# Performance work log

Measured on AMD Instinct MI355X. Metric: run time of the kernel, lower is better.

## Reference

```python
import jax, jax.numpy as jnp
import numpy as np
from math import ceil

B, T, FQ, D = 2, 48, 100, 512
H, DFF, L, WSZ = 8, 2048, 6, 8


def setup_inputs() -> dict:
    key = jax.random.key(0)
    ks = jax.random.split(key, 8)
    g = lambda k, shape: jax.random.normal(k, shape, jnp.float32) * 0.02
    return {
        "frame_queries": jax.random.normal(ks[0], (B, T, FQ, D), jnp.float32),
        "Wp": g(ks[1], (D, D)), "bp": jnp.zeros((D,), jnp.float32),
        "Wqkv": g(ks[2], (L, 3 * D, D)), "bqkv": jnp.zeros((L, 3 * D), jnp.float32),
        "Wo": g(ks[3], (L, D, D)), "bo": jnp.zeros((L, D), jnp.float32),
        "ln1_s": jnp.ones((L, D), jnp.float32), "ln1_b": jnp.zeros((L, D), jnp.float32),
        "W1": g(ks[4], (L, DFF, D)), "b1": jnp.zeros((L, DFF), jnp.float32),
        "W2": g(ks[5], (L, D, DFF)), "b2": jnp.zeros((L, D), jnp.float32),
        "ln2_s": jnp.ones((L, D), jnp.float32), "ln2_b": jnp.zeros((L, D), jnp.float32),
    }


def _ln(x, s, b, eps=1e-5):
    mu = x.mean(-1, keepdims=True)
    var = ((x - mu) ** 2).mean(-1, keepdims=True)
    return (x - mu) * jax.lax.rsqrt(var + eps) * s + b


def _mha(x, Wqkv_i, bqkv_i, Wo_i, bo_i, add_mask):
    # x: [Bw, S, C]; add_mask: None or [Bw, 1, S, S] additive float
    Bw, S, C = x.shape
    hd = C // H
    qkv = x @ Wqkv_i.T + bqkv_i
    q, k, v = jnp.split(qkv, 3, axis=-1)
    q = q.reshape(Bw, S, H, hd).transpose(0, 2, 1, 3)
    k = k.reshape(Bw, S, H, hd).transpose(0, 2, 1, 3)
    v = v.reshape(Bw, S, H, hd).transpose(0, 2, 1, 3)
    scores = jnp.einsum('bhqd,bhkd->bhqk', q, k) * jnp.float32(1.0 / np.sqrt(hd))
    if add_mask is not None:
        scores = scores + add_mask
    a = jax.nn.softmax(scores, axis=-1)
    o = jnp.einsum('bhqk,bhkd->bhqd', a, v).transpose(0, 2, 1, 3).reshape(Bw, S, C)
    return o @ Wo_i.T + bo_i


def _shift_mask():
    # padding mask is all-False (T % WSZ == 0), faithful construction of the
    # shifted-window additive mask as in the torch code.
    Nw = T // WSZ
    half = int(ceil(WSZ / 2))
    S = WSZ * FQ
    am = jnp.zeros((B, T), dtype=bool)
    r = jnp.roll(am, half, axis=1).reshape(B, Nw, WSZ)
    m = jnp.broadcast_to(r[..., None], (B, Nw, WSZ, WSZ))
    m = m.at[:, 0].set(m[:, 0] | m[:, 0].swapaxes(-1, -2))
    m = m.at[:, -1].set(m[:, -1] | m[:, -1].swapaxes(-1, -2))
    m = m.at[:, 0, :half, half:].set(True)
    m = m.at[:, 0, half:, :half].set(True)
    mfull = jnp.broadcast_to(m.reshape(B * Nw, WSZ, 1, WSZ, 1),
                             (B * Nw, WSZ, FQ, WSZ, FQ)).reshape(B * Nw, S, S)
    return (mfull.astype(jnp.float32) * -1000.0)[:, None]  # [B*Nw,1,S,S]


def reference(frame_queries, Wp, bp, Wqkv, bqkv, Wo, bo, ln1_s, ln1_b,
              W1, b1, W2, b2, ln2_s, ln2_b):
    Nw = T // WSZ
    half = int(ceil(WSZ / 2))
    S = WSZ * FQ
    x = frame_queries @ Wp.T + bp  # [B, T, FQ, D]
    shift_add = _shift_mask()
    for i in range(L):
        if i % 2 == 0:
            # plain window attention
            xw = x.reshape(B * Nw, S, D)
            xw = _ln(xw + _mha(xw, Wqkv[i], bqkv[i], Wo[i], bo[i], None),
                     ln1_s[i], ln1_b[i])
            x = xw.reshape(B, T, FQ, D)
        else:
            # shifted window attention
            xs = jnp.roll(x, half, axis=1)
            xw = xs.reshape(B * Nw, S, D)
            xw = _ln(xw + _mha(xw, Wqkv[i], bqkv[i], Wo[i], bo[i], shift_add),
                     ln1_s[i], ln1_b[i])
            x = jnp.roll(xw.reshape(B, T, FQ, D), -half, axis=1)
        # FFN (pointwise over channel dim)
        h = jax.nn.relu(x @ W1[i].T + b1[i]) @ W2[i].T + b2[i]
        x = _ln(x + h, ln2_s[i], ln2_b[i])
    return x  # [B, T, FQ, D] == 'lb t nq c'
```

## Files before the change

### kernel.cpp

```cpp
#include <hip/hip_runtime.h>


typedef float  f4    __attribute__((ext_vector_type(4)));
typedef __bf16 bf8   __attribute__((ext_vector_type(8)));
typedef unsigned short u16x8 __attribute__((ext_vector_type(8)));
typedef unsigned short u16x4 __attribute__((ext_vector_type(4)));

__device__ __forceinline__ unsigned short f2bf(float f) {
    unsigned int u = __builtin_bit_cast(unsigned int, f);
    u += 0x7fffu + ((u >> 16) & 1u);
    return (unsigned short)(u >> 16);
}
__device__ __forceinline__ float bf2f(unsigned short s) {
    return __builtin_bit_cast(float, ((unsigned int)s) << 16);
}

#define GLD16(gp, lp) __builtin_amdgcn_global_load_lds( \
    (const __attribute__((address_space(1))) void*)(gp), \
    (__attribute__((address_space(3))) void*)(lp), 16, 0, 0)

__device__ __forceinline__ int map_row(int r, int rshift) {
    if (!rshift) return r;
    int bb = r / 4800, rem = r % 4800;
    int tt = rem / 100, f = rem - tt * 100;
    return bb * 4800 + ((tt + rshift) % 48) * 100 + f;
}

template<int BM>
__global__ __launch_bounds__(256) void mfma_gemm(
    const unsigned short* __restrict__ A, const unsigned short* __restrict__ W,
    const float* __restrict__ bias, float* Cf, unsigned short* Cb,
    int M, int N, int K, int relu, int rshift, int qscale, int NB)
{
    constexpr int MI      = BM / 32;
    constexpr int ABUF    = BM * 32;
    constexpr int SB      = ABUF + 4096;
    constexpr int AROUNDS = BM / 64;
    __shared__ unsigned short Ls[3 * SB];
    const int tid = threadIdx.x, lane = tid & 63, wave = tid >> 6;

    const int per = gridDim.x >> 3;
    const int l = (blockIdx.x & 7) * per + (blockIdx.x >> 3);
    if (l >= NB * (M / BM)) return;
    const int n0 = (l % NB) * 128, m0 = (l / NB) * BM;

    const unsigned short* ga[AROUNDS];
    #pragma unroll
    for (int it = 0; it < AROUNDS; ++it) {
        int s = it * 256 + tid, row = s >> 2, cg = (s & 3) ^ ((row >> 1) & 3);
        ga[it] = A + (size_t)map_row(m0 + row, rshift) * K + cg * 8;
    }
    const unsigned short* gb[2];
    #pragma unroll
    for (int it = 0; it < 2; ++it) {
        int s = it * 256 + tid, row = s >> 2, cg = (s & 3) ^ ((row >> 1) & 3);
        gb[it] = W + (size_t)(n0 + row) * K + cg * 8;
    }

    const int wm = (wave >> 1) * (BM / 2), wn = (wave & 1) * 64;
    const int lr = lane & 15, quad = lane >> 4;

    auto STAGE = [&](int kt2, int buf) {
        const int k1 = kt2 << 5;
        unsigned short* Lb = &Ls[buf * SB];
        #pragma unroll
        for (int it = 0; it < AROUNDS; ++it)
            GLD16(ga[it] + k1, &Lb[(it * 256 + wave * 64) * 8]);
        #pragma unroll
        for (int it = 0; it < 2; ++it)
            GLD16(gb[it] + k1, &Lb[ABUF + (it * 256 + wave * 64) * 8]);
    };

    f4 acc[MI][4];
    #pragma unroll
    for (int i = 0; i < MI; ++i)
        #pragma unroll
        for (int j = 0; j < 4; ++j) acc[i][j] = 0.f;

    const int NK = K >> 5;
    STAGE(0, 0);
    STAGE(1, 1);

    int cb = 0;
    for (int kt = 0; kt < NK; ++kt) {
        if (kt + 1 < NK) {
            if constexpr (BM == 128) asm volatile("s_waitcnt vmcnt(4)" ::: "memory");
            else                     asm volatile("s_waitcnt vmcnt(3)" ::: "memory");
        } else {
            asm volatile("s_waitcnt vmcnt(0)" ::: "memory");
        }
        __builtin_amdgcn_s_barrier();
        __builtin_amdgcn_sched_barrier(0);
        const int ib = (cb == 0) ? 2 : cb - 1;
        if (kt + 2 < NK) STAGE(kt + 2, ib);

        const unsigned short* Ab = &Ls[cb * SB];
        const unsigned short* Bb = &Ls[cb * SB + ABUF];
        bf8 af[MI], bfr[4];
        #pragma unroll
        for (int mi = 0; mi < MI; ++mi) {
            int m = wm + mi * 16 + lr;
            int c = quad ^ ((m >> 1) & 3);
            af[mi] = __builtin_bit_cast(bf8, *(const u16x8*)&Ab[(m * 4 + c) * 8]);
        }
        #pragma unroll
        for (int ni = 0; ni < 4; ++ni) {
            int n = wn + ni * 16 + lr;
            int c = quad ^ ((n >> 1) & 3);
            bfr[ni] = __builtin_bit_cast(bf8, *(const u16x8*)&Bb[(n * 4 + c) * 8]);
        }
        #pragma unroll
        for (int mi = 0; mi < MI; ++mi)
            #pragma unroll
            for (int ni = 0; ni < 4; ++ni)
                acc[mi][ni] = __builtin_amdgcn_mfma_f32_16x16x32_bf16(
                    af[mi], bfr[ni], acc[mi][ni], 0, 0, 0);
        __builtin_amdgcn_sched_barrier(0);
        cb = (cb + 1 == 3) ? 0 : cb + 1;
    }

    #pragma unroll
    for (int mi = 0; mi < MI; ++mi) {
        #pragma unroll
        for (int ni = 0; ni < 4; ++ni) {
            const int rowg = m0 + wm + mi * 16 + quad * 4;
            const int colg = n0 + wn + ni * 16 + lr;
            const float bv = bias[colg];
            const float sc = (qscale && colg < 512) ? 0.125f : 1.0f;
            #pragma unroll
            for (int r = 0; r < 4; ++r) {
                float v = (acc[mi][ni][r] + bv) * sc;
                if (relu) v = fmaxf(v, 0.f);
                const size_t off = (size_t)(rowg + r) * N + colg;
                if (Cf) Cf[off] = v;
                if (Cb) Cb[off] = f2bf(v);
            }
        }
    }
}

__global__ __launch_bounds__(320) void flash_attn_mfma(
    const unsigned short* __restrict__ qkv, unsigned short* __restrict__ o,
    int masked)
{
    __shared__ unsigned short Ks[2][2048];
    __shared__ unsigned short VT[2][64 * 34];
    __shared__ unsigned short Ps[5][576];

    const int bid = blockIdx.x;
    const int h = bid & 7, kk2 = bid >> 3;
    const int qt = kk2 % 10, w = kk2 / 10;
    const int tid = threadIdx.x, lane = tid & 63, wave = tid >> 6;
    const int lr = lane & 15, quad = lane >> 4;
    const int qb = qt * 80 + wave * 16;
    const size_t wbase = (size_t)w * 800 * 1536;
    const bool do_mask = masked && ((w % 6) == 0);

    bf8 aQ[2];
    {
        const unsigned short* qp =
            qkv + wbase + (size_t)(qb + lr) * 1536 + h * 64 + quad * 8;
        aQ[0] = __builtin_bit_cast(bf8, *(const u16x8*)qp);
        aQ[1] = __builtin_bit_cast(bf8, *(const u16x8*)(qp + 32));
    }

    const unsigned short* gk = qkv;
    int kw = 0;
    if (wave < 4) {
        int s = wave * 64 + lane, row = s >> 3, clog = (s & 7) ^ (row & 7);
        gk = qkv + wbase + (size_t)row * 1536 + 512 + h * 64 + clog * 8;
        kw = wave * 512;
    }
    const int vkey = tid >> 3, vd0 = (tid & 7) * 8;
    const unsigned short* gv =
        qkv + wbase + (size_t)vkey * 1536 + 1024 + h * 64 + vd0;

    float lsum = 0.f;
    f4 oacc[4];
    #pragma unroll
    for (int dt = 0; dt < 4; ++dt) oacc[dt] = 0.f;

    const bool qhl = (qb + lr) >= 400;

    if (wave < 4) GLD16(gk, &Ks[0][kw]);
    if (tid < 256) {
        u16x8 vv0 = *(const u16x8*)gv;
        #pragma unroll
        for (int j = 0; j < 8; ++j) VT[0][(vd0 + j) * 34 + vkey] = vv0[j];
    }

    for (int kt = 0; kt < 25; ++kt) {
        const int cb = kt & 1, nb = cb ^ 1;
        const int k0 = kt * 32;
        __syncthreads();

        u16x8 vv;
        const bool pf = (kt < 24);
        if (pf && wave < 4) GLD16(gk + (size_t)(k0 + 32) * 1536, &Ks[nb][kw]);
        if (pf && tid < 256) vv = *(const u16x8*)(gv + (size_t)(k0 + 32) * 1536);

        f4 st[2];
        st[0] = 0.f; st[1] = 0.f;
        #pragma unroll
        for (int kh = 0; kh < 2; ++kh) {
            const int cx = (kh * 4 + quad) ^ (lane & 7);
            bf8 kf0 = __builtin_bit_cast(bf8, *(const u16x8*)&Ks[cb][(lr * 8 + cx) * 8]);
            bf8 kf1 = __builtin_bit_cast(bf8, *(const u16x8*)&Ks[cb][((16 + lr) * 8 + cx) * 8]);
            st[0] = __builtin_amdgcn_mfma_f32_16x16x32_bf16(kf0, aQ[kh], st[0], 0, 0, 0);
            st[1] = __builtin_amdgcn_mfma_f32_16x16x32_bf16(kf1, aQ[kh], st[1], 0, 0, 0);
        }

        {
            u16x4 pk0, pk1;
            float ls = 0.f;
            #pragma unroll
            for (int r = 0; r < 4; ++r) {
                float a = st[0][r], b = st[1][r];
                if (do_mask) {
                    if (((k0 + quad * 4 + r) >= 400) != qhl)      a -= 1000.f;
                    if (((k0 + 16 + quad * 4 + r) >= 400) != qhl) b -= 1000.f;
                }
                float p0 = __expf(fminf(a, 80.f));
                float p1 = __expf(fminf(b, 80.f));
                ls += p0 + p1;
                pk0[r] = (unsigned short)(__builtin_bit_cast(unsigned int, p0) >> 16);
                pk1[r] = (unsigned short)(__builtin_bit_cast(unsigned int, p1) >> 16);
            }
            lsum += ls;
            *(u16x4*)&Ps[wave][lr * 36 + quad * 4]      = pk0;
            *(u16x4*)&Ps[wave][lr * 36 + 16 + quad * 4] = pk1;
        }

        if (pf && tid < 256) {
            #pragma unroll
            for (int j = 0; j < 8; ++j) VT[nb][(vd0 + j) * 34 + vkey] = vv[j];
        }

        bf8 aP = __builtin_bit_cast(bf8, *(const u16x8*)&Ps[wave][lr * 36 + quad * 8]);
        #pragma unroll
        for (int dt = 0; dt < 4; ++dt) {
            bf8 bV = __builtin_bit_cast(bf8,
                *(const u16x8*)&VT[cb][(dt * 16 + lr) * 34 + quad * 8]);
            oacc[dt] = __builtin_amdgcn_mfma_f32_16x16x32_bf16(aP, bV, oacc[dt], 0, 0, 0);
        }
    }

    {
        float l = lsum;
        l += __shfl_xor(l, 16);
        l += __shfl_xor(l, 32);
        float inv[4];
        #pragma unroll
        for (int r = 0; r < 4; ++r)
            inv[r] = 1.0f / __shfl(l, quad * 4 + r);
        #pragma unroll
        for (int dt = 0; dt < 4; ++dt)
            #pragma unroll
            for (int r = 0; r < 4; ++r)
                o[((size_t)w * 800 + qb + quad * 4 + r) * 512 + h * 64 + dt * 16 + lr] =
                    f2bf(oacc[dt][r] * inv[r]);
    }
}

__global__ __launch_bounds__(256) void add_ln_kernel(
    const unsigned short* xb, const unsigned short* dlt,
    const float* __restrict__ s, const float* __restrict__ b,
    float* outf, unsigned short* outb, int rshift)
{
    const int wave = threadIdx.x >> 6, lane = threadIdx.x & 63;
    const int row = blockIdx.x * 4 + wave;
    const int xrow = map_row(row, rshift);
    const int c = lane * 8;
    u16x8 xv = *(const u16x8*)(xb  + (size_t)xrow * 512 + c);
    u16x8 dv = *(const u16x8*)(dlt + (size_t)row  * 512 + c);
    f4 u0, u1;
    #pragma unroll
    for (int j = 0; j < 4; ++j) {
        u0[j] = bf2f(xv[j])     + bf2f(dv[j]);
        u1[j] = bf2f(xv[4 + j]) + bf2f(dv[4 + j]);
    }
    float sum = u0[0]+u0[1]+u0[2]+u0[3] + u1[0]+u1[1]+u1[2]+u1[3];
    #pragma unroll
    for (int o2 = 1; o2 < 64; o2 <<= 1) sum += __shfl_xor(sum, o2);
    const float mu = sum * (1.0f / 512.0f);
    f4 d0 = u0 - mu, d1 = u1 - mu;
    float sq = d0[0]*d0[0]+d0[1]*d0[1]+d0[2]*d0[2]+d0[3]*d0[3]
             + d1[0]*d1[0]+d1[1]*d1[1]+d1[2]*d1[2]+d1[3]*d1[3];
    #pragma unroll
    for (int o2 = 1; o2 < 64; o2 <<= 1) sq += __shfl_xor(sq, o2);
    const float rs = rsqrtf(sq * (1.0f / 512.0f) + 1e-5f);
    f4 s0 = *(const f4*)(s + c), s1 = *(const f4*)(s + c + 4);
    f4 b0 = *(const f4*)(b + c), b1 = *(const f4*)(b + c + 4);
    f4 y0, y1;
    #pragma unroll
    for (int j = 0; j < 4; ++j) { y0[j] = d0[j]*rs*s0[j]+b0[j]; y1[j] = d1[j]*rs*s1[j]+b1[j]; }
    u16x8 ob;
    #pragma unroll
    for (int j = 0; j < 4; ++j) { ob[j] = f2bf(y0[j]); ob[4+j] = f2bf(y1[j]); }
    *(u16x8*)(outb + (size_t)xrow * 512 + c) = ob;
    if (outf) {
        float* of = outf + (size_t)xrow * 512 + c;
        *(f4*)of = y0; *(f4*)(of + 4) = y1;
    }
}

__global__ __launch_bounds__(256) void cast_f2b_kernel(
    const float* __restrict__ in, unsigned short* __restrict__ out, int n4)
{
    const int i = blockIdx.x * 256 + threadIdx.x;
    if (i >= n4) return;
    f4 v = ((const f4*)in)[i];
    u16x4 o4 = {f2bf(v[0]), f2bf(v[1]), f2bf(v[2]), f2bf(v[3])};
    ((u16x4*)out)[i] = o4;
}

extern "C" void kernel_launch(void* const* d_in, const int* in_sizes, int n_in,
                              void* d_out, int out_size, void* d_ws, size_t ws_size,
                              hipStream_t stream)
{
    const float* fq   = (const float*)d_in[0];
    const float* Wp   = (const float*)d_in[1];
    const float* bp   = (const float*)d_in[2];
    const float* Wqkv = (const float*)d_in[3];
    const float* bqkv = (const float*)d_in[4];
    const float* Wo   = (const float*)d_in[5];
    const float* bo   = (const float*)d_in[6];
    const float* l1s  = (const float*)d_in[7];
    const float* l1b  = (const float*)d_in[8];
    const float* W1   = (const float*)d_in[9];
    const float* b1   = (const float*)d_in[10];
    const float* W2   = (const float*)d_in[11];
    const float* b2   = (const float*)d_in[12];
    const float* l2s  = (const float*)d_in[13];
    const float* l2b  = (const float*)d_in[14];
    float* out = (float*)d_out;

    unsigned short* xb   = (unsigned short*)d_ws;
    unsigned short* qkvb = xb + 4915200;
    unsigned short* hbuf = qkvb + 14745600;
    unsigned short* wbuf = hbuf + 19660800;
    unsigned short* obuf = hbuf;
    unsigned short* t1b  = qkvb;
    unsigned short* fqb  = hbuf;
    unsigned short* wqA = wbuf;
    unsigned short* woA = wqA + 4718592;
    unsigned short* w1A = woA + 1572864;
    unsigned short* w2A = w1A + 6291456;
    unsigned short* wpA = w2A + 6291456;

    const dim3 blk(256);
    #define G8(n) dim3((((n) + 7) & ~7))
    cast_f2b_kernel<<<dim3(4800), blk, 0, stream>>>(fq,   fqb, 1228800);
    cast_f2b_kernel<<<dim3(4608), blk, 0, stream>>>(Wqkv, wqA, 1179648);
    cast_f2b_kernel<<<dim3(1536), blk, 0, stream>>>(Wo,   woA, 393216);
    cast_f2b_kernel<<<dim3(6144), blk, 0, stream>>>(W1,   w1A, 1572864);
    cast_f2b_kernel<<<dim3(6144), blk, 0, stream>>>(W2,   w2A, 1572864);
    cast_f2b_kernel<<<dim3(256),  blk, 0, stream>>>(Wp,   wpA, 65536);
    mfma_gemm<64><<<G8(600), blk, 0, stream>>>(fqb, wpA, bp, nullptr, xb,
                                               9600, 512, 512, 0, 0, 0, 4);

    for (int i = 0; i < 6; ++i) {
        const int rsh = (i & 1) ? 44 : 0;
        const unsigned short* wq = wqA + (size_t)i * 786432;
        const unsigned short* wo = woA + (size_t)i * 262144;
        const unsigned short* w1 = w1A + (size_t)i * 1048576;
        const unsigned short* w2 = w2A + (size_t)i * 1048576;
        mfma_gemm<128><<<G8(900), blk, 0, stream>>>(xb, wq, bqkv + i * 1536,
                                                    nullptr, qkvb, 9600, 1536, 512, 0, rsh, 1, 12);
        flash_attn_mfma<<<dim3(960), dim3(320), 0, stream>>>(qkvb, obuf, i & 1);
        mfma_gemm<64><<<G8(600), blk, 0, stream>>>(obuf, wo, bo + i * 512,
                                                   nullptr, t1b, 9600, 512, 512, 0, 0, 0, 4);
        add_ln_kernel<<<dim3(2400), blk, 0, stream>>>(xb, t1b, l1s + i * 512, l1b + i * 512,
                                                      nullptr, xb, rsh);
        mfma_gemm<128><<<G8(1200), blk, 0, stream>>>(xb, w1, b1 + i * 2048,
                                                     nullptr, hbuf, 9600, 2048, 512, 1, 0, 0, 16);
        mfma_gemm<64><<<G8(600), blk, 0, stream>>>(hbuf, w2, b2 + i * 512,
                                                   nullptr, t1b, 9600, 512, 2048, 0, 0, 0, 4);
        add_ln_kernel<<<dim3(2400), blk, 0, stream>>>(xb, t1b, l2s + i * 512, l2b + i * 512,
                                                      (i == 5) ? out : nullptr, xb, 0);
    }
    #undef G8
}
```

Measured before the change: 1.190 ms.

## Add BK=64 double-buffered GEMM for FFN and raise MFMA priority in attention

Adds a new GEMM kernel with a K-tile of 64, a two-stage LDS double buffer, an 8-way XOR swizzle and a plain 2D grid. It replaces the triple-buffered BK=32 kernel for the two FFN GEMMs, halving the number of K iterations and barriers per tile. The flash attention kernel also wraps its MFMA sections in s_setprio so matrix work gets issue priority over other waves. The larger LDS footprint may reduce occupancy, and dropping the XCD-aware block remap may hurt cache locality.

Result: no change. 1.191 ms (+0.1%).

```diff
diff --git a/kernel.cpp b/kernel.cpp
--- a/kernel.cpp
+++ b/kernel.cpp
@@ -41,7 +41,8 @@
 
     const int per = gridDim.x >> 3;
     const int l = (blockIdx.x & 7) * per + (blockIdx.x >> 3);
-    if (l >= NB * (M / BM)) return;
+    const int MB = M / BM;
+    if (l >= NB * MB) return;
     const int n0 = (l % NB) * 128, m0 = (l / NB) * BM;
 
     const unsigned short* ga[AROUNDS];
@@ -117,6 +118,108 @@
                     af[mi], bfr[ni], acc[mi][ni], 0, 0, 0);
         __builtin_amdgcn_sched_barrier(0);
         cb = (cb + 1 == 3) ? 0 : cb + 1;
+    }
+
+    #pragma unroll
+    for (int mi = 0; mi < MI; ++mi) {
+        #pragma unroll
+        for (int ni = 0; ni < 4; ++ni) {
+            const int rowg = m0 + wm + mi * 16 + quad * 4;
+            const int colg = n0 + wn + ni * 16 + lr;
+            const float bv = bias[colg];
+            const float sc = (qscale && colg < 512) ? 0.125f : 1.0f;
+            #pragma unroll
+            for (int r = 0; r < 4; ++r) {
+                float v = (acc[mi][ni][r] + bv) * sc;
+                if (relu) v = fmaxf(v, 0.f);
+                const size_t off = (size_t)(rowg + r) * N + colg;
+                if (Cf) Cf[off] = v;
+                if (Cb) Cb[off] = f2bf(v);
+            }
+        }
+    }
+}
+
+template<int BM>
+__global__ __launch_bounds__(256) void gemm_bk64(
+    const unsigned short* __restrict__ A, const unsigned short* __restrict__ W,
+    const float* __restrict__ bias, float* Cf, unsigned short* Cb,
+    int M, int N, int K, int relu, int rshift, int qscale)
+{
+    constexpr int MI      = BM / 32;
+    constexpr int ABUF    = BM * 64;
+    constexpr int AROUNDS = BM / 32;
+    __shared__ unsigned short As[2 * ABUF];
+    __shared__ unsigned short Bs[2 * 8192];
+    const int tid = threadIdx.x, lane = tid & 63, wave = tid >> 6;
+    const int n0 = blockIdx.x * 128, m0 = blockIdx.y * BM;
+
+    const unsigned short* ga[AROUNDS];
+    unsigned short* la[AROUNDS];
+    #pragma unroll
+    for (int it = 0; it < AROUNDS; ++it) {
+        int s = it * 256 + tid, row = s >> 3, cg = (s & 7) ^ (row & 7);
+        ga[it] = A + (size_t)map_row(m0 + row, rshift) * K + cg * 8;
+        la[it] = &As[(it * 256 + wave * 64) * 8];
+    }
+    const unsigned short* gb[4];
+    unsigned short* lb[4];
+    #pragma unroll
+    for (int it = 0; it < 4; ++it) {
+        int s = it * 256 + tid, row = s >> 3, cg = (s & 7) ^ (row & 7);
+        gb[it] = W + (size_t)(n0 + row) * K + cg * 8;
+        lb[it] = &Bs[(it * 256 + wave * 64) * 8];
+    }
+
+    const int wm = (wave >> 1) * (BM / 2), wn = (wave & 1) * 64;
+    const int lr = lane & 15, quad = lane >> 4;
+
+    f4 acc[MI][4];
+    #pragma unroll
+    for (int i = 0; i < MI; ++i)
+        #pragma unroll
+        for (int j = 0; j < 4; ++j) acc[i][j] = 0.f;
+
+    #pragma unroll
+    for (int it = 0; it < AROUNDS; ++it) GLD16(ga[it], la[it]);
+    #pragma unroll
+    for (int it = 0; it < 4; ++it) GLD16(gb[it], lb[it]);
+
+    const int NK = K >> 6;
+    for (int kt = 0; kt < NK; ++kt) {
+        const int cb = kt & 1, nb = cb ^ 1;
+        __syncthreads();
+        if (kt + 1 < NK) {
+            const int k1 = (kt + 1) << 6;
+            #pragma unroll
+            for (int it = 0; it < AROUNDS; ++it) GLD16(ga[it] + k1, la[it] + nb * ABUF);
+            #pragma unroll
+            for (int it = 0; it < 4; ++it)       GLD16(gb[it] + k1, lb[it] + nb * 8192);
+        }
+        const unsigned short* Ab = &As[cb * ABUF];
+        const unsigned short* Bb = &Bs[cb * 8192];
+        #pragma unroll
+        for (int kh = 0; kh < 2; ++kh) {
+            bf8 af[MI], bfr[4];
+            #pragma unroll
+            for (int mi = 0; mi < MI; ++mi) {
+                int m = wm + mi * 16 + lr;
+                int c = (kh * 4 + quad) ^ (m & 7);
+                af[mi] = __builtin_bit_cast(bf8, *(const u16x8*)&Ab[(m * 8 + c) * 8]);
+            }
+            #pragma unroll
+            for (int ni = 0; ni < 4; ++ni) {
+                int n = wn + ni * 16 + lr;
+                int c = (kh * 4 + quad) ^ (n & 7);
+                bfr[ni] = __builtin_bit_cast(bf8, *(const u16x8*)&Bb[(n * 8 + c) * 8]);
+            }
+            #pragma unroll
+            for (int mi = 0; mi < MI; ++mi)
+                #pragma unroll
+                for (int ni = 0; ni < 4; ++ni)
+                    acc[mi][ni] = __builtin_amdgcn_mfma_f32_16x16x32_bf16(
+                        af[mi], bfr[ni], acc[mi][ni], 0, 0, 0);
+        }
     }
 
     #pragma unroll
@@ -201,6 +304,7 @@
 
         f4 st[2];
         st[0] = 0.f; st[1] = 0.f;
+        __builtin_amdgcn_s_setprio(1);
         #pragma unroll
         for (int kh = 0; kh < 2; ++kh) {
             const int cx = (kh * 4 + quad) ^ (lane & 7);
@@ -209,6 +313,7 @@
             st[0] = __builtin_amdgcn_mfma_f32_16x16x32_bf16(kf0, aQ[kh], st[0], 0, 0, 0);
             st[1] = __builtin_amdgcn_mfma_f32_16x16x32_bf16(kf1, aQ[kh], st[1], 0, 0, 0);
         }
+        __builtin_amdgcn_s_setprio(0);
 
         {
             u16x4 pk0, pk1;
@@ -237,12 +342,14 @@
         }
 
         bf8 aP = __builtin_bit_cast(bf8, *(const u16x8*)&Ps[wave][lr * 36 + quad * 8]);
+        __builtin_amdgcn_s_setprio(1);
         #pragma unroll
         for (int dt = 0; dt < 4; ++dt) {
             bf8 bV = __builtin_bit_cast(bf8,
                 *(const u16x8*)&VT[cb][(dt * 16 + lr) * 34 + quad * 8]);
             oacc[dt] = __builtin_amdgcn_mfma_f32_16x16x32_bf16(aP, bV, oacc[dt], 0, 0, 0);
         }
+        __builtin_amdgcn_s_setprio(0);
     }
 
     {
@@ -372,10 +479,10 @@
                                                    nullptr, t1b, 9600, 512, 512, 0, 0, 0, 4);
         add_ln_kernel<<<dim3(2400), blk, 0, stream>>>(xb, t1b, l1s + i * 512, l1b + i * 512,
                                                       nullptr, xb, rsh);
-        mfma_gemm<128><<<G8(1200), blk, 0, stream>>>(xb, w1, b1 + i * 2048,
-                                                     nullptr, hbuf, 9600, 2048, 512, 1, 0, 0, 16);
-        mfma_gemm<64><<<G8(600), blk, 0, stream>>>(hbuf, w2, b2 + i * 512,
-                                                   nullptr, t1b, 9600, 512, 2048, 0, 0, 0, 4);
+        gemm_bk64<128><<<dim3(16, 75), blk, 0, stream>>>(xb, w1, b1 + i * 2048,
+                                                         nullptr, hbuf, 9600, 2048, 512, 1, 0, 0);
+        gemm_bk64<64><<<dim3(4, 150), blk, 0, stream>>>(hbuf, w2, b2 + i * 512,
+                                                        nullptr, t1b, 9600, 512, 2048, 0, 0, 0);
         add_ln_kernel<<<dim3(2400), blk, 0, stream>>>(xb, t1b, l2s + i * 512, l2b + i * 512,
                                                       (i == 5) ? out : nullptr, xb, 0);
     }
```
